# Optimization experiments

Hardware: AMD Instinct MI355X
Metric: run time of the kernel (lower is better)

Reference implementation:

```python
import jax, jax.numpy as jnp
import numpy as np
from jax import lax

H = 12  # num_heads

def conv1d_same(x, w, b):
    # x: [B, Cin, L], w: [Cout, Cin, K] (torch Conv1d layout), 'same' padding
    y = lax.conv_general_dilated(x, w, window_strides=(1,), padding='SAME',
                                 dimension_numbers=('NCH', 'OIH', 'NCH'))
    return y + b[None, :, None]

def setup_inputs() -> dict:
    key = jax.random.key(0)
    ks = jax.random.split(key, 16)
    B, N, C = 8, 4096, 768
    d = C // H
    s = 0.02
    return {
        'x': jax.random.normal(ks[0], (B, N, C), dtype=jnp.float32),
        'qkv_w': jax.random.normal(ks[1], (3 * C, C), dtype=jnp.float32) * s,
        'proj_w': jax.random.normal(ks[2], (C, C), dtype=jnp.float32) * s,
        'proj_b': jnp.zeros((C,), dtype=jnp.float32),
        'conv_w': jax.random.normal(ks[3], (d, d, 5), dtype=jnp.float32) * s,  # k=5 from log2(768)
        'conv_b': jnp.zeros((d,), dtype=jnp.float32),
        'fc_w': jax.random.normal(ks[4], (d, d), dtype=jnp.float32) * s,
        'fc_b': jnp.zeros((d,), dtype=jnp.float32),
        'dw1_w': jax.random.normal(ks[5], (d, d, 3), dtype=jnp.float32) * s,
        'dw1_b': jnp.zeros((d,), dtype=jnp.float32),
        'dw2_w': jax.random.normal(ks[6], (d, d, 5), dtype=jnp.float32) * s,
        'dw2_b': jnp.zeros((d,), dtype=jnp.float32),
    }

def reference(x, qkv_w, proj_w, proj_b, conv_w, conv_b, fc_w, fc_b, dw1_w, dw1_b, dw2_w, dw2_b):
    B, N, C = x.shape
    d = C // H
    scale = d ** (-0.5)
    # qkv projection -> [3, B, H, N, d]
    qkv = (x @ qkv_w.T).reshape(B, N, 3, H, d).transpose(2, 0, 3, 1, 4)
    q, k, v = qkv[0], qkv[1], qkv[2]
    # SE-style gate: global avg over tokens, conv over channel axis, sigmoid
    res = jnp.mean(v, axis=2).reshape(B * H, d, 1)          # [BH, d, 1]
    res = conv1d_same(res, conv_w, conv_b)                   # [BH, d, 1]
    res = jax.nn.sigmoid(res).transpose(0, 2, 1).reshape(B, H, 1, d)
    # value branch: two 1D convs over token axis (channels = head_dim)
    vch = v.reshape(B * H, N, d).transpose(0, 2, 1)          # [BH, d, N]
    v2 = conv1d_same(vch, dw1_w, dw1_b) + conv1d_same(vch, dw2_w, dw2_b)
    v2 = v2.transpose(0, 2, 1).reshape(B, H, N, d)
    # channel attention: (scaled k)^T @ q -> [B, H, d, d]
    kq = jnp.einsum('bhnd,bhne->bhde', k * scale, q)
    a = jax.nn.relu(kq) @ fc_w.T + fc_b
    a = jax.nn.softmax(a + kq, axis=-1)
    # (a @ v2^T)^T -> [B, H, N, d]
    out = jnp.einsum('bhde,bhne->bhnd', a, v2)
    out = res * out
    out = out.transpose(0, 2, 1, 3).reshape(B, N, C)
    return out @ proj_w.T + proj_b
```

## Files before the change

### kernel.cpp

```cpp
#include <hip/hip_runtime.h>
#include <hip/hip_bf16.h>
#include <cstdint>
#include <cstddef>

typedef unsigned short u16;
typedef __attribute__((ext_vector_type(4))) unsigned short u16x4;
typedef __attribute__((ext_vector_type(8))) unsigned short u16x8;
typedef __attribute__((ext_vector_type(8))) short bf16x8;
typedef __attribute__((ext_vector_type(4))) float f32x4;

#define BB 8
#define NN 4096
#define CC 768
#define HH 12
#define DD 64
#define NHEADS 96
#define QKVSZ 25165824LL

__device__ inline float b2f(u16 u) { return __uint_as_float(((unsigned)u) << 16); }
__device__ inline u16 f2b(float f) {
    unsigned u = __float_as_uint(f);
    return (u16)((u + 0x7fffu + ((u >> 16) & 1u)) >> 16);
}
__device__ inline f32x4 zero4() { f32x4 z = {0.f, 0.f, 0.f, 0.f}; return z; }

__device__ __forceinline__ void gl_lds16(const u16* g, u16* l) {
    __builtin_amdgcn_global_load_lds(
        (const __attribute__((address_space(1))) void*)g,
        (__attribute__((address_space(3))) void*)l, 16, 0, 0);
}

__global__ void cast_f32_bf16(const float* __restrict__ src, u16* __restrict__ dst, int n) {
    long i0 = (long)(blockIdx.x * blockDim.x + threadIdx.x) * 4;
    long stride = (long)gridDim.x * blockDim.x * 4;
    for (long j = i0; j < n; j += stride) {
        float4 v = *(const float4*)(src + j);
        u16x4 o;
        o[0] = f2b(v.x); o[1] = f2b(v.y); o[2] = f2b(v.z); o[3] = f2b(v.w);
        *(u16x4*)(dst + j) = o;
    }
}

template <int MODE>
__global__ __launch_bounds__(256) void gemm128d(const u16* __restrict__ A, const u16* __restrict__ Bm,
                                                const float* __restrict__ bias, void* __restrict__ out,
                                                int ncol) {
    constexpr int K = 768;
    __shared__ __align__(16) u16 lA[128 * 64];
    __shared__ __align__(16) u16 lB[128 * 64];
    const int tid = threadIdx.x;
    const int lane = tid & 63, wid = tid >> 6;
    const int wr = wid >> 1, wc = wid & 1;
    const int li = lane & 15, g = lane >> 4;

    const int nwg = gridDim.x, chunk = nwg >> 3;
    const int swz = ((int)blockIdx.x & 7) * chunk + ((int)blockIdx.x >> 3);
    const int col0 = (swz % ncol) * 128;
    const int row0 = (swz / ncol) * 128;

    const int lrow = lane >> 3;
    const int lcolsw = (((lane & 7) ^ lrow) * 8);

    f32x4 acc[4][4];
#pragma unroll
    for (int i = 0; i < 4; ++i)
#pragma unroll
        for (int j = 0; j < 4; ++j) acc[i][j] = zero4();

    for (int kt = 0; kt < K; kt += 64) {
#pragma unroll
        for (int s = 0; s < 4; ++s) {
            int r0 = wid * 32 + s * 8;
            gl_lds16(A  + (size_t)(row0 + r0 + lrow) * K + kt + lcolsw, lA + r0 * 64);
            gl_lds16(Bm + (size_t)(col0 + r0 + lrow) * K + kt + lcolsw, lB + r0 * 64);
        }
        __syncthreads();
#pragma unroll
        for (int kk = 0; kk < 64; kk += 32) {
            int kc = kk * 2 + (g << 4);
            bf16x8 af[4], bf_[4];
#pragma unroll
            for (int i = 0; i < 4; ++i) {
                int ra = wr * 64 + i * 16 + li;
                af[i] = *(const bf16x8*)((char*)lA + ((ra * 128 + kc) ^ ((ra & 7) << 4)));
                int rb = wc * 64 + i * 16 + li;
                bf_[i] = *(const bf16x8*)((char*)lB + ((rb * 128 + kc) ^ ((rb & 7) << 4)));
            }
#pragma unroll
            for (int i = 0; i < 4; ++i)
#pragma unroll
                for (int j = 0; j < 4; ++j)
                    acc[i][j] = __builtin_amdgcn_mfma_f32_16x16x32_bf16(af[i], bf_[j], acc[i][j], 0, 0, 0);
        }
        __syncthreads();
    }

#pragma unroll
    for (int i = 0; i < 4; ++i) {
#pragma unroll
        for (int j = 0; j < 4; ++j) {
            int c = col0 + wc * 64 + j * 16 + li;
            if constexpr (MODE == 0) {
                int part = c / 768, rem = c % 768;
                int h = rem >> 6, dd = rem & 63;
#pragma unroll
                for (int e = 0; e < 4; ++e) {
                    int r = row0 + wr * 64 + i * 16 + g * 4 + e;
                    int b = r >> 12, n = r & 4095;
                    ((u16*)out)[(((size_t)part * NHEADS + b * HH + h) * NN + n) * DD + dd] =
                        f2b(acc[i][j][e]);
                }
            } else {
                float bb = bias[c];
#pragma unroll
                for (int e = 0; e < 4; ++e) {
                    int r = row0 + wr * 64 + i * 16 + g * 4 + e;
                    ((float*)out)[(size_t)r * 768 + c] = acc[i][j][e] + bb;
                }
            }
        }
    }
}

__global__ __launch_bounds__(256) void kq_mean(const u16* __restrict__ qkv, float* __restrict__ kqp,
                                               float* __restrict__ meanp) {
    const int head = blockIdx.x, part = blockIdx.y;
    const int tid = threadIdx.x, lane = tid & 63, wid = tid >> 6;
    __shared__ __align__(16) u16 tiles[4][2][32 * 64];
    __shared__ float sred[16 * 64];

    if (part == 4) {
        const u16* vh = qkv + 2 * QKVSZ + (size_t)head * NN * DD;
        int rg = tid >> 4, cg = tid & 15;
        float s0 = 0.f, s1 = 0.f, s2 = 0.f, s3 = 0.f;
        for (int it = 0; it < 256; ++it) {
            int n = rg + it * 16;
            u16x4 v = *(const u16x4*)(vh + (size_t)n * DD + cg * 4);
            s0 += b2f(v[0]); s1 += b2f(v[1]); s2 += b2f(v[2]); s3 += b2f(v[3]);
        }
        sred[rg * 64 + cg * 4 + 0] = s0;
        sred[rg * 64 + cg * 4 + 1] = s1;
        sred[rg * 64 + cg * 4 + 2] = s2;
        sred[rg * 64 + cg * 4 + 3] = s3;
        __syncthreads();
        if (tid < 64) {
            float s = 0.f;
#pragma unroll
            for (int rg2 = 0; rg2 < 16; ++rg2) s += sred[rg2 * 64 + tid];
            meanp[head * 64 + tid] = s;
        }
        return;
    }

    u16* kt = tiles[wid][0];
    u16* qt = tiles[wid][1];
    const u16* qh = qkv + (size_t)head * NN * DD;
    const u16* kh = qkv + QKVSZ + (size_t)head * NN * DD;
    const int nbase = part * 1024 + wid * 256;

    f32x4 acc[4][4];
#pragma unroll
    for (int i = 0; i < 4; ++i)
#pragma unroll
        for (int j = 0; j < 4; ++j) acc[i][j] = zero4();

    const int srow = lane >> 3, schunk = (lane & 7) * 8;
    const int g8 = (lane >> 4) * 8, li = lane & 15;

    for (int it = 0; it < 8; ++it) {
        int n0 = nbase + it * 32;
#pragma unroll
        for (int p = 0; p < 4; ++p) {
            int r = srow + p * 8;
            *(u16x8*)(kt + r * 64 + schunk) = *(const u16x8*)(kh + (size_t)(n0 + r) * DD + schunk);
            *(u16x8*)(qt + r * 64 + schunk) = *(const u16x8*)(qh + (size_t)(n0 + r) * DD + schunk);
        }
        bf16x8 af[4], bf_[4];
#pragma unroll
        for (int i = 0; i < 4; ++i)
#pragma unroll
            for (int j = 0; j < 8; ++j) af[i][j] = (short)kt[(g8 + j) * 64 + i * 16 + li];
#pragma unroll
        for (int i = 0; i < 4; ++i)
#pragma unroll
            for (int j = 0; j < 8; ++j) bf_[i][j] = (short)qt[(g8 + j) * 64 + i * 16 + li];
#pragma unroll
        for (int i = 0; i < 4; ++i)
#pragma unroll
            for (int j = 0; j < 4; ++j)
                acc[i][j] = __builtin_amdgcn_mfma_f32_16x16x32_bf16(af[i], bf_[j], acc[i][j], 0, 0, 0);
    }

    const int slot = part * 4 + wid;
    const int g = lane >> 4;
    float* dst = kqp + ((size_t)head * 16 + slot) * 4096;
#pragma unroll
    for (int i = 0; i < 4; ++i)
#pragma unroll
        for (int j = 0; j < 4; ++j)
#pragma unroll
            for (int e = 0; e < 4; ++e)
                dst[(i * 16 + g * 4 + e) * 64 + j * 16 + li] = acc[i][j][e];
}

__global__ __launch_bounds__(256) void head_finish(
    const float* __restrict__ kqp, const float* __restrict__ meanp,
    const float* __restrict__ conv_w, const float* __restrict__ conv_b,
    const float* __restrict__ fc_w, const float* __restrict__ fc_b,
    const float* __restrict__ dw1_w, const float* __restrict__ dw1_b,
    const float* __restrict__ dw2_w, const float* __restrict__ dw2_b,
    u16* __restrict__ eff, float* __restrict__ effb) {
    const int head = blockIdx.x;
    const int tid = threadIdx.x;
    __shared__ float skq[64 * 64];
    __shared__ float sa[64 * 64];
    __shared__ float sgate[64];
    __shared__ float sw2[64 * 16 * 5];
    __shared__ float sw1[64 * 16 * 3];

    for (int idx = tid; idx < 4096; idx += 256) {
        float s = 0.f;
#pragma unroll
        for (int p = 0; p < 16; ++p) s += kqp[((size_t)head * 16 + p) * 4096 + idx];
        skq[idx] = s * 0.125f;
    }
    __syncthreads();
    if (tid < 64) {
        float gsum = conv_b[tid];
        for (int i = 0; i < 64; ++i)
            gsum += conv_w[(tid * 64 + i) * 5 + 2] * (meanp[head * 64 + i] * (1.f / 4096.f));
        sgate[tid] = 1.f / (1.f + __expf(-gsum));
    }

    {
        int rr = tid >> 2, cg = (tid & 3) * 16;
        for (int c = cg; c < cg + 16; ++c) {
            float s = fc_b[c];
            for (int e = 0; e < 64; ++e) s += fmaxf(skq[rr * 64 + e], 0.f) * fc_w[c * 64 + e];
            sa[rr * 64 + c] = s + skq[rr * 64 + c];
        }
    }
    __syncthreads();
    if (tid < 64) {
        float m = -1e30f;
        for (int e = 0; e < 64; ++e) m = fmaxf(m, sa[tid * 64 + e]);
        float s = 0.f;
        for (int e = 0; e < 64; ++e) {
            float p = __expf(sa[tid * 64 + e] - m);
            sa[tid * 64 + e] = p;
            s += p;
        }
        float inv = 1.f / s;
        for (int e = 0; e < 64; ++e) sa[tid * 64 + e] *= inv;
    }
    __syncthreads();
    if (tid < 64) {
        float s = 0.f;
        for (int e = 0; e < 64; ++e) s += sa[tid * 64 + e] * (dw1_b[e] + dw2_b[e]);
        effb[head * 64 + tid] = sgate[tid] * s;
    }

    for (int ig = 0; ig < 4; ++ig) {
        __syncthreads();
        for (int idx = tid; idx < 64 * 16 * 5; idx += 256) {
            int e = idx / 80, rem = idx % 80, il2 = rem / 5, t = rem % 5;
            sw2[idx] = dw2_w[((size_t)(e * 64 + ig * 16 + il2)) * 5 + t];
        }
        for (int idx = tid; idx < 64 * 16 * 3; idx += 256) {
            int e = idx / 48, rem = idx % 48, il2 = rem / 3, t = rem % 3;
            sw1[idx] = dw1_w[((size_t)(e * 64 + ig * 16 + il2)) * 3 + t];
        }
        __syncthreads();

        const int il = tid & 15, og = tid >> 4;
        const int i = ig * 16 + il;
        float t[4][5];
#pragma unroll
        for (int o = 0; o < 4; ++o)
#pragma unroll
            for (int tp = 0; tp < 5; ++tp) t[o][tp] = 0.f;

        for (int e = 0; e < 64; ++e) {
            float a0 = sa[(og * 4 + 0) * 64 + e];
            float a1 = sa[(og * 4 + 1) * 64 + e];
            float a2 = sa[(og * 4 + 2) * 64 + e];
            float a3 = sa[(og * 4 + 3) * 64 + e];
            const float* w2 = sw2 + (e * 16 + il) * 5;
            const float* w1 = sw1 + (e * 16 + il) * 3;
            float c0 = w2[0], c1 = w2[1] + w1[0], c2 = w2[2] + w1[1], c3 = w2[3] + w1[2], c4 = w2[4];
            t[0][0] += a0 * c0; t[0][1] += a0 * c1; t[0][2] += a0 * c2; t[0][3] += a0 * c3; t[0][4] += a0 * c4;
            t[1][0] += a1 * c0; t[1][1] += a1 * c1; t[1][2] += a1 * c2; t[1][3] += a1 * c3; t[1][4] += a1 * c4;
            t[2][0] += a2 * c0; t[2][1] += a2 * c1; t[2][2] += a2 * c2; t[2][3] += a2 * c3; t[2][4] += a2 * c4;
            t[3][0] += a3 * c0; t[3][1] += a3 * c1; t[3][2] += a3 * c2; t[3][3] += a3 * c3; t[3][4] += a3 * c4;
        }
#pragma unroll
        for (int o = 0; o < 4; ++o) {
            int oo = og * 4 + o;
            float gt = sgate[oo];
            u16* eo = eff + ((size_t)head * 64 + oo) * 320 + i;
#pragma unroll
            for (int tp = 0; tp < 5; ++tp) eo[tp * 64] = f2b(gt * t[o][tp]);
        }
    }
}

__global__ __launch_bounds__(256) void conv_attn(const u16* __restrict__ qkv, const u16* __restrict__ eff,
                                                 const float* __restrict__ effb, u16* __restrict__ attn) {
    const int nt = blockIdx.x, head = blockIdx.y;
    const int tid = threadIdx.x, lane = tid & 63, wid = tid >> 6;
    __shared__ __align__(16) u16 vt[132 * 64];
    const int n0 = nt * 128;
    const u16* vh = qkv + 2 * QKVSZ + (size_t)head * NN * DD;

    {
        int sr = tid >> 3, sc = (tid & 7) * 8;
#pragma unroll
        for (int p = 0; p < 5; ++p) {
            int r = sr + p * 32;
            if (r < 132) {
                int n = n0 - 2 + r;
                u16x8 v = {0, 0, 0, 0, 0, 0, 0, 0};
                if (n >= 0 && n < NN) v = *(const u16x8*)(vh + (size_t)n * DD + sc);
                *(u16x8*)((char*)vt + ((r * 128 + sc * 2) ^ ((r & 7) << 4))) = v;
            }
        }
    }
    __syncthreads();

    f32x4 acc[2][4];
#pragma unroll
    for (int s = 0; s < 2; ++s)
#pragma unroll
        for (int j = 0; j < 4; ++j) acc[s][j] = zero4();

    const u16* effh = eff + (size_t)head * 64 * 320;
    const int li = lane & 15, g = lane >> 4;
#pragma unroll
    for (int s = 0; s < 10; ++s) {
        int tap = s >> 1, half = s & 1;
        bf16x8 bfr[4];
#pragma unroll
        for (int nj = 0; nj < 4; ++nj)
            bfr[nj] = *(const bf16x8*)(effh + (size_t)(nj * 16 + li) * 320 + s * 32 + g * 8);
        int kc = half * 64 + g * 16;
#pragma unroll
        for (int sub = 0; sub < 2; ++sub) {
            int rr = wid * 32 + sub * 16 + li + tap;
            bf16x8 afr = *(const bf16x8*)((char*)vt + ((rr * 128 + kc) ^ ((rr & 7) << 4)));
#pragma unroll
            for (int nj = 0; nj < 4; ++nj)
                acc[sub][nj] = __builtin_amdgcn_mfma_f32_16x16x32_bf16(afr, bfr[nj], acc[sub][nj], 0, 0, 0);
        }
    }

    const int b = head / HH, h = head % HH;
#pragma unroll
    for (int sub = 0; sub < 2; ++sub)
#pragma unroll
        for (int nj = 0; nj < 4; ++nj) {
            int o = nj * 16 + li;
            float bb = effb[head * 64 + o];
#pragma unroll
            for (int e = 0; e < 4; ++e) {
                int m = wid * 32 + sub * 16 + g * 4 + e;
                size_t n = (size_t)n0 + m;
                attn[((size_t)b * NN + n) * CC + h * DD + o] = f2b(acc[sub][nj][e] + bb);
            }
        }
}

extern "C" void kernel_launch(void* const* d_in, const int* in_sizes, int n_in,
                              void* d_out, int out_size, void* d_ws, size_t ws_size,
                              hipStream_t stream) {
    const float* x      = (const float*)d_in[0];
    const float* qkv_w  = (const float*)d_in[1];
    const float* proj_w = (const float*)d_in[2];
    const float* proj_b = (const float*)d_in[3];
    const float* conv_w = (const float*)d_in[4];
    const float* conv_b = (const float*)d_in[5];
    const float* fc_w   = (const float*)d_in[6];
    const float* fc_b   = (const float*)d_in[7];
    const float* dw1_w  = (const float*)d_in[8];
    const float* dw1_b  = (const float*)d_in[9];
    const float* dw2_w  = (const float*)d_in[10];
    const float* dw2_b  = (const float*)d_in[11];

    char* ws = (char*)d_ws;
    u16* xb    = (u16*)(ws);
    u16* wqkv  = (u16*)(ws + 50331648);
    u16* wproj = (u16*)(ws + 53870592);
    u16* qkv   = (u16*)(ws + 55050240);
    u16* eff   = (u16*)(ws + 206045184);
    float* effb = (float*)(ws + 209977344);
    u16* attn  = (u16*)(ws + 210001920);

    float* kqp   = (float*)(ws);
    float* meanp = (float*)(ws + 25165824);

    float* out = (float*)d_out;

    cast_f32_bf16<<<1024, 256, 0, stream>>>(x, xb, BB * NN * CC);
    cast_f32_bf16<<<256, 256, 0, stream>>>(qkv_w, wqkv, 3 * CC * CC);
    cast_f32_bf16<<<256, 256, 0, stream>>>(proj_w, wproj, CC * CC);

    gemm128d<0><<<4608, 256, 0, stream>>>(xb, wqkv, nullptr, qkv, 18);

    kq_mean<<<dim3(96, 5), 256, 0, stream>>>(qkv, kqp, meanp);
    head_finish<<<96, 256, 0, stream>>>(kqp, meanp, conv_w, conv_b, fc_w, fc_b,
                                        dw1_w, dw1_b, dw2_w, dw2_b, eff, effb);

    conv_attn<<<dim3(32, 96), 256, 0, stream>>>(qkv, eff, effb, attn);

    gemm128d<1><<<1536, 256, 0, stream>>>(attn, wproj, proj_b, out, 6);
}
```

Measured before the change: 429.7 us.

## Double-buffer GEMM LDS tiles with K=32 steps and fuse cast kernels

```diff
diff --git a/kernel.cpp b/kernel.cpp
--- a/kernel.cpp
+++ b/kernel.cpp
@@ -30,24 +30,32 @@
         (__attribute__((address_space(3))) void*)l, 16, 0, 0);
 }
 
-__global__ void cast_f32_bf16(const float* __restrict__ src, u16* __restrict__ dst, int n) {
+__global__ void cast_all(const float* __restrict__ x, const float* __restrict__ w1,
+                         const float* __restrict__ w2, u16* __restrict__ xb,
+                         u16* __restrict__ wqkv, u16* __restrict__ wproj) {
+    const long n0 = 25165824, n1 = 1769472, n2 = 589824;
     long i0 = (long)(blockIdx.x * blockDim.x + threadIdx.x) * 4;
     long stride = (long)gridDim.x * blockDim.x * 4;
-    for (long j = i0; j < n; j += stride) {
-        float4 v = *(const float4*)(src + j);
+    for (long j = i0; j < n0 + n1 + n2; j += stride) {
+        const float* s; u16* d; long k;
+        if (j < n0)            { s = x;  d = xb;    k = j; }
+        else if (j < n0 + n1)  { s = w1; d = wqkv;  k = j - n0; }
+        else                   { s = w2; d = wproj; k = j - n0 - n1; }
+        float4 v = *(const float4*)(s + k);
         u16x4 o;
         o[0] = f2b(v.x); o[1] = f2b(v.y); o[2] = f2b(v.z); o[3] = f2b(v.w);
-        *(u16x4*)(dst + j) = o;
+        *(u16x4*)(d + k) = o;
     }
 }
 
 template <int MODE>
-__global__ __launch_bounds__(256) void gemm128d(const u16* __restrict__ A, const u16* __restrict__ Bm,
+__global__ __launch_bounds__(256) void gemm128e(const u16* __restrict__ A, const u16* __restrict__ Bm,
                                                 const float* __restrict__ bias, void* __restrict__ out,
                                                 int ncol) {
     constexpr int K = 768;
-    __shared__ __align__(16) u16 lA[128 * 64];
-    __shared__ __align__(16) u16 lB[128 * 64];
+    constexpr int NT = K / 32;
+    __shared__ __align__(16) u16 lA[2][128 * 32];
+    __shared__ __align__(16) u16 lB[2][128 * 32];
     const int tid = threadIdx.x;
     const int lane = tid & 63, wid = tid >> 6;
     const int wr = wid >> 1, wc = wid & 1;
@@ -58,8 +66,8 @@
     const int col0 = (swz % ncol) * 128;
     const int row0 = (swz / ncol) * 128;
 
-    const int lrow = lane >> 3;
-    const int lcolsw = (((lane & 7) ^ lrow) * 8);
+    const int srow = lane >> 2;
+    const int scol = ((lane & 3) ^ ((lane >> 3) & 3)) * 8;
 
     f32x4 acc[4][4];
 #pragma unroll
@@ -67,32 +75,40 @@
 #pragma unroll
         for (int j = 0; j < 4; ++j) acc[i][j] = zero4();
 
-    for (int kt = 0; kt < K; kt += 64) {
-#pragma unroll
-        for (int s = 0; s < 4; ++s) {
-            int r0 = wid * 32 + s * 8;
-            gl_lds16(A  + (size_t)(row0 + r0 + lrow) * K + kt + lcolsw, lA + r0 * 64);
-            gl_lds16(Bm + (size_t)(col0 + r0 + lrow) * K + kt + lcolsw, lB + r0 * 64);
-        }
+    const int r0s = wid * 32;
+
+    gl_lds16(A  + (size_t)(row0 + r0s +      srow) * K + scol, &lA[0][ r0s       * 32]);
+    gl_lds16(A  + (size_t)(row0 + r0s + 16 + srow) * K + scol, &lA[0][(r0s + 16) * 32]);
+    gl_lds16(Bm + (size_t)(col0 + r0s +      srow) * K + scol, &lB[0][ r0s       * 32]);
+    gl_lds16(Bm + (size_t)(col0 + r0s + 16 + srow) * K + scol, &lB[0][(r0s + 16) * 32]);
+
+    int buf = 0;
+    for (int t = 0; t < NT; ++t) {
         __syncthreads();
-#pragma unroll
-        for (int kk = 0; kk < 64; kk += 32) {
-            int kc = kk * 2 + (g << 4);
-            bf16x8 af[4], bf_[4];
-#pragma unroll
-            for (int i = 0; i < 4; ++i) {
-                int ra = wr * 64 + i * 16 + li;
-                af[i] = *(const bf16x8*)((char*)lA + ((ra * 128 + kc) ^ ((ra & 7) << 4)));
-                int rb = wc * 64 + i * 16 + li;
-                bf_[i] = *(const bf16x8*)((char*)lB + ((rb * 128 + kc) ^ ((rb & 7) << 4)));
-            }
-#pragma unroll
-            for (int i = 0; i < 4; ++i)
-#pragma unroll
-                for (int j = 0; j < 4; ++j)
-                    acc[i][j] = __builtin_amdgcn_mfma_f32_16x16x32_bf16(af[i], bf_[j], acc[i][j], 0, 0, 0);
-        }
-        __syncthreads();
+        if (t + 1 < NT) {
+            const int kt = (t + 1) * 32;
+            const int nb = buf ^ 1;
+            gl_lds16(A  + (size_t)(row0 + r0s +      srow) * K + kt + scol, &lA[nb][ r0s       * 32]);
+            gl_lds16(A  + (size_t)(row0 + r0s + 16 + srow) * K + kt + scol, &lA[nb][(r0s + 16) * 32]);
+            gl_lds16(Bm + (size_t)(col0 + r0s +      srow) * K + kt + scol, &lB[nb][ r0s       * 32]);
+            gl_lds16(Bm + (size_t)(col0 + r0s + 16 + srow) * K + kt + scol, &lB[nb][(r0s + 16) * 32]);
+        }
+        bf16x8 af[4], bf_[4];
+#pragma unroll
+        for (int i = 0; i < 4; ++i) {
+            int ra = wr * 64 + i * 16 + li;
+            af[i] = *(const bf16x8*)((const char*)&lA[buf][0] +
+                                     ra * 64 + ((g ^ ((ra >> 1) & 3)) << 4));
+            int rb = wc * 64 + i * 16 + li;
+            bf_[i] = *(const bf16x8*)((const char*)&lB[buf][0] +
+                                      rb * 64 + ((g ^ ((rb >> 1) & 3)) << 4));
+        }
+#pragma unroll
+        for (int i = 0; i < 4; ++i)
+#pragma unroll
+            for (int j = 0; j < 4; ++j)
+                acc[i][j] = __builtin_amdgcn_mfma_f32_16x16x32_bf16(af[i], bf_[j], acc[i][j], 0, 0, 0);
+        buf ^= 1;
     }
 
 #pragma unroll
@@ -399,11 +415,9 @@
 
     float* out = (float*)d_out;
 
-    cast_f32_bf16<<<1024, 256, 0, stream>>>(x, xb, BB * NN * CC);
-    cast_f32_bf16<<<256, 256, 0, stream>>>(qkv_w, wqkv, 3 * CC * CC);
-    cast_f32_bf16<<<256, 256, 0, stream>>>(proj_w, wproj, CC * CC);
-
-    gemm128d<0><<<4608, 256, 0, stream>>>(xb, wqkv, nullptr, qkv, 18);
+    cast_all<<<2048, 256, 0, stream>>>(x, qkv_w, proj_w, xb, wqkv, wproj);
+
+    gemm128e<0><<<4608, 256, 0, stream>>>(xb, wqkv, nullptr, qkv, 18);
 
     kq_mean<<<dim3(96, 5), 256, 0, stream>>>(qkv, kqp, meanp);
     head_finish<<<96, 256, 0, stream>>>(kqp, meanp, conv_w, conv_b, fc_w, fc_b,
@@ -411,5 +425,5 @@
 
     conv_attn<<<dim3(32, 96), 256, 0, stream>>>(qkv, eff, effb, attn);
 
-    gemm128d<1><<<1536, 256, 0, stream>>>(attn, wproj, proj_b, out, 6);
-}
+    gemm128e<1><<<1536, 256, 0, stream>>>(attn, wproj, proj_b, out, 6);
+}
```

New measurement: 460.2 us. 1.07x slower.
